# Kernel optimization log

Measured on AMD Instinct MI355X. Metric: run time of the kernel, lower is better.

Reference implementation:

```python
import jax, jax.numpy as jnp
import numpy as np

D, P, R, K = 1024, 256, 64, 1024  # directions, sampling points, rank, subcarriers

def setup_inputs() -> dict:
    key = jax.random.key(0)
    k1, k2, k3 = jax.random.split(key, 3)
    return {
        "attenuation_vectors": jax.random.normal(k1, (D, P, R), dtype=jnp.float32),
        "radiation_vectors": jax.random.normal(k2, (D, P, R), dtype=jnp.float32),
        "frequency_basis_vectors": jax.random.normal(k3, (K, R), dtype=jnp.float32),
    }

def reference(attenuation_vectors, radiation_vectors, frequency_basis_vectors):
    # Original (per ray d, per subcarrier k):
    #   atten_factor[d,k] = sum_p sum_r u_rho[d,p,r] * F[k,r]
    #   rad_factor[d,k]   = sum_p sum_r u_s[d,p,r]   * F[k,r]
    #   csi[k] = (1/D) * sum_d atten_factor[d,k] * rad_factor[d,k]
    # Vectorized as two contractions over (p, r) plus a reduction over d.
    A = jnp.einsum('dpr,kr->dk', attenuation_vectors, frequency_basis_vectors)
    B = jnp.einsum('dpr,kr->dk', radiation_vectors, frequency_basis_vectors)
    num_directions = attenuation_vectors.shape[0]
    csi = jnp.sum(A * B, axis=0) / num_directions  # [K]
    return csi
```

## Files before the change

kernel.cpp:

```cpp
#include <hip/hip_runtime.h>

#define D_DIRS 1024
#define P_PTS  256
#define R_RANK 64
#define K_SUB  1024

typedef float v4f __attribute__((ext_vector_type(4)));

#define WS_A 0
#define WS_B (D_DIRS * R_RANK)
#define WS_M (2 * D_DIRS * R_RANK)
#define WS_MSUM 0
#define NB_B 32
#define DCHUNK (D_DIRS / NB_B)

__device__ __forceinline__ v4f ntload(const v4f* __restrict__ p) {
    return __builtin_nontemporal_load(p);
}

__global__ __launch_bounds__(512) void k_reduce_p(const float* __restrict__ atten,
                                                  const float* __restrict__ rad,
                                                  float* __restrict__ ws) {
    const int d     = blockIdx.x;
    const int t     = threadIdx.x;
    const int rq    = t & 15;
    const int pg    = t >> 4;
    const int phase = d & 7;

    const v4f* A4 = (const v4f*)atten + (size_t)d * (P_PTS * R_RANK / 4);
    const v4f* B4 = (const v4f*)rad   + (size_t)d * (P_PTS * R_RANK / 4);

    v4f va[8], vb[8];
#pragma unroll
    for (int k = 0; k < 8; ++k) {
        const int kk  = (k + phase) & 7;
        const int idx = (pg + (kk << 5)) * 16 + rq;
        va[k] = ntload(A4 + idx);
    }
#pragma unroll
    for (int k = 0; k < 8; ++k) {
        const int kk  = (k + phase) & 7;
        const int idx = (pg + (kk << 5)) * 16 + rq;
        vb[k] = ntload(B4 + idx);
    }

    v4f sa = (va[0] + va[1]) + (va[2] + va[3]) + ((va[4] + va[5]) + (va[6] + va[7]));
    v4f sb = (vb[0] + vb[1]) + (vb[2] + vb[3]) + ((vb[4] + vb[5]) + (vb[6] + vb[7]));

    __shared__ v4f ra[32][16];
    __shared__ v4f rb[32][16];
    ra[pg][rq] = sa;
    rb[pg][rq] = sb;
    __syncthreads();
#pragma unroll
    for (int s = 16; s >= 1; s >>= 1) {
        if (pg < s) {
            ra[pg][rq] = ra[pg][rq] + ra[pg + s][rq];
            rb[pg][rq] = rb[pg][rq] + rb[pg + s][rq];
        }
        __syncthreads();
    }
    if (t < 16) {
        v4f* a4 = (v4f*)(ws + WS_A);
        v4f* b4 = (v4f*)(ws + WS_B);
        a4[d * 16 + t] = ra[0][t];
        b4[d * 16 + t] = rb[0][t];
    }
}

__global__ __launch_bounds__(256) void k_partial_m(float* __restrict__ ws) {
    const int bb = blockIdx.x;
    const int t  = threadIdx.x;

    __shared__ float sa[DCHUNK * R_RANK];
    __shared__ float sb[DCHUNK * R_RANK];

    const float4* a4 = (const float4*)(ws + WS_A) + bb * (DCHUNK * R_RANK / 4);
    const float4* b4 = (const float4*)(ws + WS_B) + bb * (DCHUNK * R_RANK / 4);
    float4* sa4 = (float4*)sa;
    float4* sb4 = (float4*)sb;
    sa4[t]       = a4[t];
    sa4[t + 256] = a4[t + 256];
    sb4[t]       = b4[t];
    sb4[t + 256] = b4[t + 256];
    __syncthreads();

    const int c  = t & 63;
    const int wg = t >> 6;

    float acc[16];
#pragma unroll
    for (int i = 0; i < 16; ++i) acc[i] = 0.f;

    for (int dd = 0; dd < DCHUNK; ++dd) {
        const float bv = sb[dd * 64 + c];
        const float4* ar = (const float4*)&sa[dd * 64 + wg * 16];
        const float4 a0 = ar[0], a1 = ar[1], a2 = ar[2], a3 = ar[3];
        acc[0]  += a0.x * bv; acc[1]  += a0.y * bv; acc[2]  += a0.z * bv; acc[3]  += a0.w * bv;
        acc[4]  += a1.x * bv; acc[5]  += a1.y * bv; acc[6]  += a1.z * bv; acc[7]  += a1.w * bv;
        acc[8]  += a2.x * bv; acc[9]  += a2.y * bv; acc[10] += a2.z * bv; acc[11] += a2.w * bv;
        acc[12] += a3.x * bv; acc[13] += a3.y * bv; acc[14] += a3.z * bv; acc[15] += a3.w * bv;
    }

    float* Mp = ws + WS_M + bb * 4096;
#pragma unroll
    for (int i = 0; i < 16; ++i) Mp[(wg * 16 + i) * 64 + c] = acc[i];
}

__global__ __launch_bounds__(256) void k_reduce_m(float* __restrict__ ws) {
    const int tg = blockIdx.x * 256 + threadIdx.x;
    const float4* Mp4 = (const float4*)(ws + WS_M);
    float4 s = make_float4(0.f, 0.f, 0.f, 0.f);
#pragma unroll
    for (int g = 0; g < NB_B; ++g) {
        const float4 v = Mp4[g * 1024 + tg];
        s.x += v.x; s.y += v.y; s.z += v.z; s.w += v.w;
    }
    ((float4*)(ws + WS_MSUM))[tg] = s;
}

__global__ __launch_bounds__(256) void k_csi(const float* __restrict__ ws,
                                             const float* __restrict__ freq,
                                             float* __restrict__ out) {
    const int bb = blockIdx.x;
    const int t  = threadIdx.x;

    __shared__ float Ms[64 * 68];
    __shared__ float Fs[64 * 65];
    __shared__ float red[4][64];

    const float4* M4 = (const float4*)(ws + WS_MSUM);
#pragma unroll
    for (int i = 0; i < 4; ++i) {
        const int idx4 = i * 256 + t;
        const float4 s = M4[idx4];
        const int r = idx4 >> 4, c4 = idx4 & 15;
        *(float4*)&Ms[r * 68 + c4 * 4] = s;
    }

    const float4* F4 = (const float4*)freq + bb * 1024;
#pragma unroll
    for (int i = 0; i < 4; ++i) {
        const int idx4 = i * 256 + t;
        const float4 v = F4[idx4];
        const int row = idx4 >> 4, c4 = idx4 & 15;
        Fs[row * 65 + c4 * 4 + 0] = v.x;
        Fs[row * 65 + c4 * 4 + 1] = v.y;
        Fs[row * 65 + c4 * 4 + 2] = v.z;
        Fs[row * 65 + c4 * 4 + 3] = v.w;
    }
    __syncthreads();

    const int kl = t & 63;
    const int jg = t >> 6;

    float h[16];
#pragma unroll
    for (int j = 0; j < 16; ++j) h[j] = 0.f;

    for (int r = 0; r < 64; ++r) {
        const float fv = Fs[kl * 65 + r];
        const float4* mr = (const float4*)&Ms[r * 68 + jg * 16];
        const float4 m0 = mr[0], m1 = mr[1], m2 = mr[2], m3 = mr[3];
        h[0]  += fv * m0.x; h[1]  += fv * m0.y; h[2]  += fv * m0.z; h[3]  += fv * m0.w;
        h[4]  += fv * m1.x; h[5]  += fv * m1.y; h[6]  += fv * m1.z; h[7]  += fv * m1.w;
        h[8]  += fv * m2.x; h[9]  += fv * m2.y; h[10] += fv * m2.z; h[11] += fv * m2.w;
        h[12] += fv * m3.x; h[13] += fv * m3.y; h[14] += fv * m3.z; h[15] += fv * m3.w;
    }

    float part = 0.f;
#pragma unroll
    for (int j = 0; j < 16; ++j) part += h[j] * Fs[kl * 65 + jg * 16 + j];

    red[jg][kl] = part;
    __syncthreads();
    if (t < 64) {
        out[bb * 64 + t] =
            (red[0][t] + red[1][t] + red[2][t] + red[3][t]) * (1.0f / (float)D_DIRS);
    }
}

extern "C" void kernel_launch(void* const* d_in, const int* in_sizes, int n_in,
                              void* d_out, int out_size, void* d_ws, size_t ws_size,
                              hipStream_t stream) {
    const float* atten = (const float*)d_in[0];
    const float* rad   = (const float*)d_in[1];
    const float* freq  = (const float*)d_in[2];
    float* out = (float*)d_out;
    float* ws  = (float*)d_ws;

    k_reduce_p<<<D_DIRS, 512, 0, stream>>>(atten, rad, ws);
    k_partial_m<<<NB_B, 256, 0, stream>>>(ws);
    k_reduce_m<<<4, 256, 0, stream>>>(ws);
    k_csi<<<16, 256, 0, stream>>>(ws, freq, out);
}
```

Before: 150.7 us.

## Process four directions per block with register prefetch and wave-shuffle reduction

```diff
diff --git a/kernel.cpp b/kernel.cpp
--- a/kernel.cpp
+++ b/kernel.cpp
@@ -18,53 +18,86 @@
     return __builtin_nontemporal_load(p);
 }
 
+__device__ __forceinline__ v4f shfl_xor_v4(v4f v, int m) {
+    v4f r;
+    r.x = __shfl_xor(v.x, m);
+    r.y = __shfl_xor(v.y, m);
+    r.z = __shfl_xor(v.z, m);
+    r.w = __shfl_xor(v.w, m);
+    return r;
+}
+
 __global__ __launch_bounds__(512) void k_reduce_p(const float* __restrict__ atten,
                                                   const float* __restrict__ rad,
                                                   float* __restrict__ ws) {
-    const int d     = blockIdx.x;
-    const int t     = threadIdx.x;
-    const int rq    = t & 15;
-    const int pg    = t >> 4;
-    const int phase = d & 7;
-
-    const v4f* A4 = (const v4f*)atten + (size_t)d * (P_PTS * R_RANK / 4);
-    const v4f* B4 = (const v4f*)rad   + (size_t)d * (P_PTS * R_RANK / 4);
-
-    v4f va[8], vb[8];
-#pragma unroll
-    for (int k = 0; k < 8; ++k) {
-        const int kk  = (k + phase) & 7;
-        const int idx = (pg + (kk << 5)) * 16 + rq;
-        va[k] = ntload(A4 + idx);
-    }
-#pragma unroll
-    for (int k = 0; k < 8; ++k) {
-        const int kk  = (k + phase) & 7;
-        const int idx = (pg + (kk << 5)) * 16 + rq;
-        vb[k] = ntload(B4 + idx);
-    }
-
-    v4f sa = (va[0] + va[1]) + (va[2] + va[3]) + ((va[4] + va[5]) + (va[6] + va[7]));
-    v4f sb = (vb[0] + vb[1]) + (vb[2] + vb[3]) + ((vb[4] + vb[5]) + (vb[6] + vb[7]));
-
-    __shared__ v4f ra[32][16];
-    __shared__ v4f rb[32][16];
-    ra[pg][rq] = sa;
-    rb[pg][rq] = sb;
-    __syncthreads();
-#pragma unroll
-    for (int s = 16; s >= 1; s >>= 1) {
-        if (pg < s) {
-            ra[pg][rq] = ra[pg][rq] + ra[pg + s][rq];
-            rb[pg][rq] = rb[pg][rq] + rb[pg + s][rq];
+    const int bid  = blockIdx.x;
+    const int t    = threadIdx.x;
+    const int lane = t & 63;
+    const int wave = t >> 6;
+    const int rq   = t & 15;
+
+    const v4f* A4 = (const v4f*)atten;
+    const v4f* B4 = (const v4f*)rad;
+
+    __shared__ v4f lA[2][8][16];
+    __shared__ v4f lB[2][8][16];
+
+    const int d0 = bid * 4;
+
+    v4f a_cur[8], b_cur[8], a_nxt[8], b_nxt[8];
+    {
+        const v4f* pa = A4 + (size_t)d0 * 4096 + t;
+        const v4f* pb = B4 + (size_t)d0 * 4096 + t;
+#pragma unroll
+        for (int k = 0; k < 8; ++k) a_cur[k] = ntload(pa + k * 512);
+#pragma unroll
+        for (int k = 0; k < 8; ++k) b_cur[k] = ntload(pb + k * 512);
+    }
+
+#pragma unroll
+    for (int dd = 0; dd < 4; ++dd) {
+        const int d = d0 + dd;
+
+        if (dd < 3) {
+            const v4f* na = A4 + (size_t)(d + 1) * 4096 + t;
+            const v4f* nb = B4 + (size_t)(d + 1) * 4096 + t;
+#pragma unroll
+            for (int k = 0; k < 8; ++k) a_nxt[k] = ntload(na + k * 512);
+#pragma unroll
+            for (int k = 0; k < 8; ++k) b_nxt[k] = ntload(nb + k * 512);
+        }
+
+        v4f sa = ((a_cur[0] + a_cur[1]) + (a_cur[2] + a_cur[3])) +
+                 ((a_cur[4] + a_cur[5]) + (a_cur[6] + a_cur[7]));
+        v4f sb = ((b_cur[0] + b_cur[1]) + (b_cur[2] + b_cur[3])) +
+                 ((b_cur[4] + b_cur[5]) + (b_cur[6] + b_cur[7]));
+
+        sa = sa + shfl_xor_v4(sa, 16);
+        sa = sa + shfl_xor_v4(sa, 32);
+        sb = sb + shfl_xor_v4(sb, 16);
+        sb = sb + shfl_xor_v4(sb, 32);
+
+        if ((lane >> 4) == 0) {
+            lA[dd & 1][wave][rq] = sa;
+            lB[dd & 1][wave][rq] = sb;
         }
         __syncthreads();
-    }
-    if (t < 16) {
-        v4f* a4 = (v4f*)(ws + WS_A);
-        v4f* b4 = (v4f*)(ws + WS_B);
-        a4[d * 16 + t] = ra[0][t];
-        b4[d * 16 + t] = rb[0][t];
+
+        if (t < 16) {
+            v4f s = lA[dd & 1][0][t];
+#pragma unroll
+            for (int w = 1; w < 8; ++w) s = s + lA[dd & 1][w][t];
+            ((v4f*)(ws + WS_A))[d * 16 + t] = s;
+        } else if (t >= 64 && t < 80) {
+            const int q = t - 64;
+            v4f s = lB[dd & 1][0][q];
+#pragma unroll
+            for (int w = 1; w < 8; ++w) s = s + lB[dd & 1][w][q];
+            ((v4f*)(ws + WS_B))[d * 16 + q] = s;
+        }
+
+#pragma unroll
+        for (int k = 0; k < 8; ++k) { a_cur[k] = a_nxt[k]; b_cur[k] = b_nxt[k]; }
     }
 }
 
@@ -189,7 +222,7 @@
     float* out = (float*)d_out;
     float* ws  = (float*)d_ws;
 
-    k_reduce_p<<<D_DIRS, 512, 0, stream>>>(atten, rad, ws);
+    k_reduce_p<<<D_DIRS / 4, 512, 0, stream>>>(atten, rad, ws);
     k_partial_m<<<NB_B, 256, 0, stream>>>(ws);
     k_reduce_m<<<4, 256, 0, stream>>>(ws);
     k_csi<<<16, 256, 0, stream>>>(ws, freq, out);
```

Result: no change. 153.7 us (+2.0%).
